# Kernel optimization log

Measured on AMD Instinct MI355X. Metric: run time of the kernel, lower is better.

Reference implementation:

```python
import jax, jax.numpy as jnp
import numpy as np

N_NODES = 100000
N_EDGES = 1600000
C_IN = 128
C_HID = 128
C_OUT = 128


def _gcn_conv(x, row, col, ew, W, b, n_nodes):
    # PyG GCNConv with edge weights and self-loops already included in (row, col, ew).
    # deg[i] = sum of edge weights into node i (flow source->target, aggregate at col)
    xw = x @ W                                                # [N, C_out]
    deg = jax.ops.segment_sum(ew, col, num_segments=n_nodes)  # [N]
    dinv = jnp.where(deg > 0, jax.lax.rsqrt(deg), 0.0)        # deg^{-1/2}, inf -> 0
    norm = dinv[row] * ew * dinv[col]                         # [E]
    msg = xw[row] * norm[:, None]                             # gather + scale
    out = jax.ops.segment_sum(msg, col, num_segments=n_nodes) # scatter-add
    return out + b


def setup_inputs() -> dict:
    key = jax.random.key(0)
    ks = jax.random.split(key, 10)
    x = jax.random.normal(ks[0], (N_NODES, C_IN), dtype=jnp.float32)
    edge_index = jax.random.randint(ks[1], (2, N_EDGES), 0, N_NODES, dtype=jnp.int32)
    edge_weight = jax.random.uniform(ks[2], (N_EDGES,), dtype=jnp.float32)
    s = 1.0 / np.sqrt(C_HID)
    W1 = jax.random.uniform(ks[3], (C_IN, C_HID), minval=-s, maxval=s, dtype=jnp.float32)
    b1 = jnp.zeros((C_HID,), dtype=jnp.float32)
    W2 = jax.random.uniform(ks[4], (C_HID, C_HID), minval=-s, maxval=s, dtype=jnp.float32)
    b2 = jnp.zeros((C_HID,), dtype=jnp.float32)
    W3 = jax.random.uniform(ks[5], (C_HID, C_OUT), minval=-s, maxval=s, dtype=jnp.float32)
    b3 = jnp.zeros((C_OUT,), dtype=jnp.float32)
    return {"x": x, "edge_index": edge_index, "edge_weight": edge_weight,
            "W1": W1, "b1": b1, "W2": W2, "b2": b2, "W3": W3, "b3": b3}


def reference(x, edge_index, edge_weight, W1, b1, W2, b2, W3, b3):
    n = x.shape[0]
    # add self-loops with weight 1 (PyG add_self_loops; identical each layer, built once)
    loop = jnp.arange(n, dtype=edge_index.dtype)
    row = jnp.concatenate([edge_index[0], loop])
    col = jnp.concatenate([edge_index[1], loop])
    ew = jnp.concatenate([edge_weight, jnp.ones((n,), dtype=edge_weight.dtype)])
    h = _gcn_conv(x, row, col, ew, W1, b1, n)
    h = jax.nn.relu(h)
    h = _gcn_conv(h, row, col, ew, W2, b2, n)
    h = jax.nn.relu(h)
    h = _gcn_conv(h, row, col, ew, W3, b3, n)
    return h
```

## Files before the change

### kernel.cpp

```cpp
#include <hip/hip_runtime.h>

#define NN 100000
#define NE 1600000

typedef __attribute__((ext_vector_type(8))) short short8;
typedef __attribute__((ext_vector_type(4))) float f32x4;

static __device__ __forceinline__ unsigned f2bf_rne(float f) {
    unsigned u = __float_as_uint(f);
    return (u + 0x7FFFu + ((u >> 16) & 1u)) >> 16;
}
static __device__ __forceinline__ float bf_lo(unsigned u) { return __uint_as_float(u << 16); }
static __device__ __forceinline__ float bf_hi(unsigned u) { return __uint_as_float(u & 0xFFFF0000u); }

__global__ __launch_bounds__(256) void k_pre(unsigned long long* packed, int n,
                                             const float* __restrict__ W1,
                                             const float* __restrict__ W2,
                                             const float* __restrict__ W3,
                                             ushort* __restrict__ wt) {
    int b = blockIdx.x;
    int t = threadIdx.x;
    if (b < 391) {
        int i = b * 256 + t;
        if (i < n) packed[i] = 0ull;
        return;
    }
    int pb = b - 391;
    int wsel = pb >> 6;
    const float* W = (wsel == 0) ? W1 : (wsel == 1) ? W2 : W3;
    ushort* Wth = wt + wsel * 2 * 16384;
    ushort* Wtl = Wth + 16384;
    int idx = (pb & 63) * 256 + t;
    int k = idx >> 7, nn = idx & 127;
    float w = W[idx];
    unsigned hi = f2bf_rne(w);
    unsigned lo = f2bf_rne(w - bf_lo(hi));
    Wth[nn * 128 + k] = (ushort)hi;
    Wtl[nn * 128 + k] = (ushort)lo;
}

template <bool SPLIT_A>
static __device__ __forceinline__ void mfma_tile(const ushort* sAh, const ushort* sAl,
                                                 const ushort* __restrict__ Wth,
                                                 const ushort* __restrict__ Wtl,
                                                 unsigned* __restrict__ Cb,
                                                 size_t r0, int t) {
    int w  = t >> 6;
    int l  = t & 63;
    int lr = l & 15;
    int lk = (l >> 4) << 3;
    int n0 = w * 32;

    short8 bh[2][4], bl[2][4];
#pragma unroll
    for (int cf = 0; cf < 2; ++cf)
#pragma unroll
        for (int ks = 0; ks < 4; ++ks) {
            int n = n0 + cf * 16 + lr;
            bh[cf][ks] = *(const short8*)&Wth[n * 128 + ks * 32 + lk];
            bl[cf][ks] = *(const short8*)&Wtl[n * 128 + ks * 32 + lk];
        }

    f32x4 zero = {0.f, 0.f, 0.f, 0.f};
    f32x4 acc[2][2] = {{zero, zero}, {zero, zero}};

    __syncthreads();

#pragma unroll
    for (int ks = 0; ks < 4; ++ks) {
        short8 ah[2], al[2];
#pragma unroll
        for (int rf = 0; rf < 2; ++rf) {
            int off = (rf * 16 + lr) * 136 + ks * 32 + lk;
            ah[rf] = *(const short8*)&sAh[off];
            if (SPLIT_A) al[rf] = *(const short8*)&sAl[off];
        }
#pragma unroll
        for (int rf = 0; rf < 2; ++rf)
#pragma unroll
            for (int cf = 0; cf < 2; ++cf) {
                acc[rf][cf] = __builtin_amdgcn_mfma_f32_16x16x32_bf16(ah[rf], bh[cf][ks], acc[rf][cf], 0, 0, 0);
                acc[rf][cf] = __builtin_amdgcn_mfma_f32_16x16x32_bf16(ah[rf], bl[cf][ks], acc[rf][cf], 0, 0, 0);
                if (SPLIT_A)
                    acc[rf][cf] = __builtin_amdgcn_mfma_f32_16x16x32_bf16(al[rf], bh[cf][ks], acc[rf][cf], 0, 0, 0);
            }
    }

#pragma unroll
    for (int rf = 0; rf < 2; ++rf)
#pragma unroll
        for (int cf = 0; cf < 2; ++cf)
#pragma unroll
            for (int r = 0; r < 4; ++r) {
                unsigned b = f2bf_rne(acc[rf][cf][r]);
                unsigned p = (unsigned)__shfl_xor((int)b, 1);
                if (!(l & 1)) {
                    size_t row = r0 + rf * 16 + ((l >> 4) << 2) + r;
                    int c = n0 + cf * 16 + lr;
                    Cb[(row * 128 + c) >> 1] = b | (p << 16);
                }
            }
}

__global__ __launch_bounds__(256) void k_gp(const float* __restrict__ A,
                                            const ushort* __restrict__ Wth,
                                            const ushort* __restrict__ Wtl,
                                            unsigned* __restrict__ Cb,
                                            const int* __restrict__ col,
                                            const float* __restrict__ ew,
                                            unsigned long long* packed,
                                            int* __restrict__ rank, int e) {
    __shared__ alignas(16) ushort sAh[32 * 136];
    __shared__ alignas(16) ushort sAl[32 * 136];
    int b = blockIdx.x;
    int sub = b % 3;
    int q = b / 3;
    int t = threadIdx.x;

    if (sub != 0) {
        int p = q * 2 + sub - 1;
        int i = p * 256 + t;
        if (i < e) {
            int c = col[i];
            unsigned fe = (unsigned)__float2uint_rn(ew[i] * 1048576.0f);
            unsigned long long inc = ((unsigned long long)fe << 24) | 1ull;
            unsigned long long old = atomicAdd(&packed[c], inc);
            rank[i] = (int)(old & 0xFFFFFFull);
        }
        return;
    }

    size_t r0 = (size_t)q * 32;
    const float4* A4 = (const float4*)(A + r0 * 128);
#pragma unroll
    for (int i = 0; i < 4; ++i) {
        int j = t + 256 * i;
        float4 f = A4[j];
        int rr = j >> 5;
        int cc = (j & 31) << 2;
        unsigned h0 = f2bf_rne(f.x), h1 = f2bf_rne(f.y), h2 = f2bf_rne(f.z), h3 = f2bf_rne(f.w);
        unsigned g0 = f2bf_rne(f.x - bf_lo(h0)), g1 = f2bf_rne(f.y - bf_lo(h1));
        unsigned g2 = f2bf_rne(f.z - bf_lo(h2)), g3 = f2bf_rne(f.w - bf_lo(h3));
        *(ushort4*)&sAh[rr * 136 + cc] = make_ushort4((ushort)h0, (ushort)h1, (ushort)h2, (ushort)h3);
        *(ushort4*)&sAl[rr * 136 + cc] = make_ushort4((ushort)g0, (ushort)g1, (ushort)g2, (ushort)g3);
    }
    mfma_tile<true>(sAh, sAl, Wth, Wtl, Cb, r0, t);
}

__global__ __launch_bounds__(256) void k_scan1(const unsigned long long* __restrict__ packed,
                                               int* __restrict__ rowptr,
                                               int* __restrict__ part,
                                               float* __restrict__ dinv, int n) {
    __shared__ int s[256];
    int t = threadIdx.x;
    int i = blockIdx.x * 256 + t;
    unsigned long long pk = (i < n) ? packed[i] : 0ull;
    int v = (int)(pk & 0xFFFFFFull);
    if (i < n) {
        float deg = 1.0f + (float)(pk >> 24) * (1.0f / 1048576.0f);
        dinv[i] = rsqrtf(deg);
    }
    s[t] = v;
    __syncthreads();
    for (int d = 1; d < 256; d <<= 1) {
        int y = (t >= d) ? s[t - d] : 0;
        __syncthreads();
        s[t] += y;
        __syncthreads();
    }
    if (i < n) rowptr[i] = s[t] - v;
    if (t == 255) part[blockIdx.x] = s[255];
}

__global__ __launch_bounds__(512) void k_scan2(int* part, int m) {
    __shared__ int s[512];
    int t = threadIdx.x;
    int v = (t < m) ? part[t] : 0;
    s[t] = v;
    __syncthreads();
    for (int d = 1; d < 512; d <<= 1) {
        int y = (t >= d) ? s[t - d] : 0;
        __syncthreads();
        s[t] += y;
        __syncthreads();
    }
    if (t < m) part[t] = s[t] - v;
}

__global__ __launch_bounds__(256) void k_scan3(int* rowptr, const int* __restrict__ part, int n, int e) {
    int i = blockIdx.x * 256 + threadIdx.x;
    if (i < n) rowptr[i] += part[blockIdx.x];
    if (i == 0) rowptr[n] = e;
}

__global__ __launch_bounds__(256) void k_fill(const int* __restrict__ row,
                                              const int* __restrict__ col,
                                              const float* __restrict__ ew,
                                              const int* __restrict__ rowptr,
                                              const int* __restrict__ rank,
                                              const float* __restrict__ dinv,
                                              uint2* __restrict__ meta, int e) {
    int i = blockIdx.x * 256 + threadIdx.x;
    if (i < e) {
        int c = col[i];
        int r = row[i];
        int p = rowptr[c] + rank[i];
        float w = dinv[r] * ew[i] * dinv[c];
        meta[p] = make_uint2((unsigned)r, __float_as_uint(w));
    }
}

static __device__ __forceinline__ void agg_node(const uint2* __restrict__ X2,
                                                const int* __restrict__ rowptr,
                                                const uint2* __restrict__ meta,
                                                const float* __restrict__ dinv,
                                                const float* __restrict__ bias,
                                                int node, int h, int q,
                                                float& a0, float& a1, float& a2, float& a3) {
    float di = dinv[node];
    float selfw = di * di;
    uint2 us = X2[(size_t)node * 32 + q];
    float4 bv = *(const float4*)(bias + q * 4);
    a0 = fmaf(selfw, bf_lo(us.x), bv.x);
    a1 = fmaf(selfw, bf_hi(us.x), bv.y);
    a2 = fmaf(selfw, bf_lo(us.y), bv.z);
    a3 = fmaf(selfw, bf_hi(us.y), bv.w);

    int p0 = rowptr[node], p1 = rowptr[node + 1];
    int deg = p1 - p0;
    int dmax = max(deg, __shfl_xor(deg, 32));

    for (int base = 0; base < dmax; base += 32) {
        int m = deg - base;
        if (m > 32) m = 32;
        int mm = dmax - base;
        if (mm > 32) mm = 32;
        int idx = p0 + base + (q < m ? q : (m > 0 ? m - 1 : 0));
        if (m <= 0) idx = p0;
        if (idx > NE - 1) idx = NE - 1;
        uint2 mv = meta[idx];
        int sv = (int)mv.x;
        float wv = __uint_as_float(mv.y);

        int j = 0;
        for (; j + 4 <= mm; j += 4) {
#pragma unroll
            for (int u = 0; u < 4; ++u) {
                int jj = j + u;
                int s = __shfl(sv, (h << 5) | jj);
                float w = __shfl(wv, (h << 5) | jj);
                w = (jj < m) ? w : 0.0f;
                uint2 u0 = X2[(size_t)s * 32 + q];
                a0 = fmaf(w, bf_lo(u0.x), a0);  a1 = fmaf(w, bf_hi(u0.x), a1);
                a2 = fmaf(w, bf_lo(u0.y), a2);  a3 = fmaf(w, bf_hi(u0.y), a3);
            }
        }
        for (; j < mm; ++j) {
            int s = __shfl(sv, (h << 5) | j);
            float w = __shfl(wv, (h << 5) | j);
            w = (j < m) ? w : 0.0f;
            uint2 u0 = X2[(size_t)s * 32 + q];
            a0 = fmaf(w, bf_lo(u0.x), a0);  a1 = fmaf(w, bf_hi(u0.x), a1);
            a2 = fmaf(w, bf_lo(u0.y), a2);  a3 = fmaf(w, bf_hi(u0.y), a3);
        }
    }
}

__global__ __launch_bounds__(256) void k_aggemm(const unsigned* __restrict__ Xsrc,
                                                const int* __restrict__ rowptr,
                                                const uint2* __restrict__ meta,
                                                const float* __restrict__ dinv,
                                                const float* __restrict__ bias,
                                                const ushort* __restrict__ Wth,
                                                const ushort* __restrict__ Wtl,
                                                unsigned* __restrict__ Cb) {
    __shared__ alignas(16) ushort sA[32 * 136];
    int t = threadIdx.x;
    int lane = t & 63, wid = t >> 6;
    int h = lane >> 5, q = lane & 31;
    const uint2* X2 = (const uint2*)Xsrc;
    size_t r0 = (size_t)blockIdx.x * 32;

#pragma unroll
    for (int p = 0; p < 4; ++p) {
        int ln = (p << 3) + (wid << 1) + h;
        int node = (int)r0 + ln;
        float a0, a1, a2, a3;
        agg_node(X2, rowptr, meta, dinv, bias, node, h, q, a0, a1, a2, a3);
        a0 = fmaxf(a0, 0.0f);  a1 = fmaxf(a1, 0.0f);
        a2 = fmaxf(a2, 0.0f);  a3 = fmaxf(a3, 0.0f);
        *(ushort4*)&sA[ln * 136 + (q << 2)] =
            make_ushort4((ushort)f2bf_rne(a0), (ushort)f2bf_rne(a1),
                         (ushort)f2bf_rne(a2), (ushort)f2bf_rne(a3));
    }
    mfma_tile<false>(sA, nullptr, Wth, Wtl, Cb, r0, t);
}

__global__ __launch_bounds__(256) void k_agg(const unsigned* __restrict__ XWb,
                                             const int* __restrict__ rowptr,
                                             const uint2* __restrict__ meta,
                                             const float* __restrict__ dinv,
                                             const float* __restrict__ bias,
                                             float* __restrict__ outf, int n) {
    int lane = threadIdx.x & 63;
    int h = lane >> 5;
    int q = lane & 31;
    int node = blockIdx.x * 8 + ((threadIdx.x >> 6) << 1) + h;
    if (node >= n) return;
    float a0, a1, a2, a3;
    agg_node((const uint2*)XWb, rowptr, meta, dinv, bias, node, h, q, a0, a1, a2, a3);
    *(float4*)(outf + (size_t)node * 128 + q * 4) = make_float4(a0, a1, a2, a3);
}

extern "C" void kernel_launch(void* const* d_in, const int* in_sizes, int n_in,
                              void* d_out, int out_size, void* d_ws, size_t ws_size,
                              hipStream_t stream) {
    const float* x  = (const float*)d_in[0];
    const int*   ei = (const int*)d_in[1];
    const float* ew = (const float*)d_in[2];
    const float* W1 = (const float*)d_in[3];
    const float* b1 = (const float*)d_in[4];
    const float* W2 = (const float*)d_in[5];
    const float* b2 = (const float*)d_in[6];
    const float* W3 = (const float*)d_in[7];
    const float* b3 = (const float*)d_in[8];
    float* out = (float*)d_out;

    const int n = NN, e = NE;
    const int* row = ei;
    const int* col = ei + e;

    char* ws = (char*)d_ws;
    size_t off = 0;
    auto alloc = [&](size_t bytes) -> void* {
        void* p = ws + off;
        off = (off + bytes + 255) & ~(size_t)255;
        return p;
    };
    unsigned*           hb     = (unsigned*)alloc((size_t)n * 128 * 2);
    unsigned*           xwb    = (unsigned*)alloc((size_t)n * 128 * 2);
    void*               uni    =            alloc((size_t)e * 8);
    unsigned long long* packed = (unsigned long long*)uni;
    uint2*              meta   = (uint2*)uni;
    float*              dinv   = (float*)   alloc((size_t)n * 4);
    int*                rowptr = (int*)     alloc((size_t)(n + 1) * 4);
    int*                rank   = (int*)     alloc((size_t)e * 4);
    int*                part   = (int*)     alloc(512 * 4);
    ushort*             wt     = (ushort*)  alloc(6 * 16384 * 2);
    (void)ws_size; (void)in_sizes; (void)n_in; (void)out_size;

    int nb = (n + 255) / 256;
    int eb = (e + 255) / 256;
    int gb = n / 32;
    int ab = (n + 7) / 8;

    k_pre<<<nb + 192, 256, 0, stream>>>(packed, n, W1, W2, W3, wt);

    k_gp<<<gb + eb, 256, 0, stream>>>(x, wt + 0 * 16384, wt + 1 * 16384, xwb, col, ew, packed, rank, e);
    k_scan1<<<nb, 256, 0, stream>>>(packed, rowptr, part, dinv, n);
    k_scan2<<<1, 512, 0, stream>>>(part, nb);
    k_scan3<<<nb, 256, 0, stream>>>(rowptr, part, n, e);
    k_fill<<<eb, 256, 0, stream>>>(row, col, ew, rowptr, rank, dinv, meta, e);

    k_aggemm<<<gb, 256, 0, stream>>>(xwb, rowptr, meta, dinv, b1,
                                     wt + 2 * 16384, wt + 3 * 16384, hb);
    k_aggemm<<<gb, 256, 0, stream>>>(hb, rowptr, meta, dinv, b2,
                                     wt + 4 * 16384, wt + 5 * 16384, xwb);
    k_agg<<<ab, 256, 0, stream>>>(xwb, rowptr, meta, dinv, b3, out, n);
}
```

Before: 478.3 us.

## Sort nodes by degree per block and aggregate four nodes per half-wave

Each block of 32 nodes now bitonic-sorts its nodes by in-degree in shared memory. Each half-wave then takes four consecutive sorted nodes and processes them together, interleaving their gathers. This is meant to cut divergence from mismatched degree loops and to keep more independent loads in flight. The separate scan3 kernel is removed: the block offset from part[] is added wherever rowptr is read, at the cost of extra indexed loads, a small sort with several syncs per block, and higher register pressure from 16 accumulators.

```diff
diff --git a/kernel.cpp b/kernel.cpp
--- a/kernel.cpp
+++ b/kernel.cpp
@@ -172,7 +172,7 @@
     if (t == 255) part[blockIdx.x] = s[255];
 }
 
-__global__ __launch_bounds__(512) void k_scan2(int* part, int m) {
+__global__ __launch_bounds__(512) void k_scan2(int* part, int m, int* rowptr, int e) {
     __shared__ int s[512];
     int t = threadIdx.x;
     int v = (t < m) ? part[t] : 0;
@@ -185,18 +185,14 @@
         __syncthreads();
     }
     if (t < m) part[t] = s[t] - v;
-}
-
-__global__ __launch_bounds__(256) void k_scan3(int* rowptr, const int* __restrict__ part, int n, int e) {
-    int i = blockIdx.x * 256 + threadIdx.x;
-    if (i < n) rowptr[i] += part[blockIdx.x];
-    if (i == 0) rowptr[n] = e;
+    if (t == m - 1) rowptr[NN] = e - (s[t] - v);
 }
 
 __global__ __launch_bounds__(256) void k_fill(const int* __restrict__ row,
                                               const int* __restrict__ col,
                                               const float* __restrict__ ew,
                                               const int* __restrict__ rowptr,
+                                              const int* __restrict__ part,
                                               const int* __restrict__ rank,
                                               const float* __restrict__ dinv,
                                               uint2* __restrict__ meta, int e) {
@@ -204,70 +200,123 @@
     if (i < e) {
         int c = col[i];
         int r = row[i];
-        int p = rowptr[c] + rank[i];
+        int p = rowptr[c] + part[c >> 8] + rank[i];
         float w = dinv[r] * ew[i] * dinv[c];
         meta[p] = make_uint2((unsigned)r, __float_as_uint(w));
     }
 }
 
-static __device__ __forceinline__ void agg_node(const uint2* __restrict__ X2,
-                                                const int* __restrict__ rowptr,
+static __device__ __forceinline__ void agg_quad(const uint2* __restrict__ X2,
                                                 const uint2* __restrict__ meta,
                                                 const float* __restrict__ dinv,
-                                                const float* __restrict__ bias,
-                                                int node, int h, int q,
-                                                float& a0, float& a1, float& a2, float& a3) {
-    float di = dinv[node];
-    float selfw = di * di;
-    uint2 us = X2[(size_t)node * 32 + q];
-    float4 bv = *(const float4*)(bias + q * 4);
-    a0 = fmaf(selfw, bf_lo(us.x), bv.x);
-    a1 = fmaf(selfw, bf_hi(us.x), bv.y);
-    a2 = fmaf(selfw, bf_lo(us.y), bv.z);
-    a3 = fmaf(selfw, bf_hi(us.y), bv.w);
-
-    int p0 = rowptr[node], p1 = rowptr[node + 1];
-    int deg = p1 - p0;
-    int dmax = max(deg, __shfl_xor(deg, 32));
-
-    for (int base = 0; base < dmax; base += 32) {
-        int m = deg - base;
-        if (m > 32) m = 32;
-        int mm = dmax - base;
-        if (mm > 32) mm = 32;
-        int idx = p0 + base + (q < m ? q : (m > 0 ? m - 1 : 0));
-        if (m <= 0) idx = p0;
-        if (idx > NE - 1) idx = NE - 1;
-        uint2 mv = meta[idx];
-        int sv = (int)mv.x;
-        float wv = __uint_as_float(mv.y);
+                                                float4 bv, int h, int q,
+                                                const int* node, const int* p0,
+                                                const int* deg, float acc[4][4]) {
+#pragma unroll
+    for (int X = 0; X < 4; ++X) {
+        float di = dinv[node[X]];
+        float sw = di * di;
+        uint2 us = X2[(size_t)node[X] * 32 + q];
+        acc[X][0] = fmaf(sw, bf_lo(us.x), bv.x);
+        acc[X][1] = fmaf(sw, bf_hi(us.x), bv.y);
+        acc[X][2] = fmaf(sw, bf_lo(us.y), bv.z);
+        acc[X][3] = fmaf(sw, bf_hi(us.y), bv.w);
+    }
+    int dloc = max(max(deg[0], deg[1]), max(deg[2], deg[3]));
+
+    for (int base = 0; base < dloc; base += 32) {
+        int m[4], idx[4];
+#pragma unroll
+        for (int X = 0; X < 4; ++X) {
+            int mx = deg[X] - base;
+            m[X] = mx > 32 ? 32 : mx;
+            int ix = p0[X] + base + (q < m[X] ? q : (m[X] > 0 ? m[X] - 1 : 0));
+            if (m[X] <= 0) ix = p0[X];
+            if (ix > NE - 1) ix = NE - 1;
+            idx[X] = ix;
+        }
+        int sv[4]; float wv[4];
+#pragma unroll
+        for (int X = 0; X < 4; ++X) {
+            uint2 mv = meta[idx[X]];
+            sv[X] = (int)mv.x;
+            wv[X] = __uint_as_float(mv.y);
+        }
+        int mmax = dloc - base;  mmax = mmax > 32 ? 32 : mmax;
 
         int j = 0;
-        for (; j + 4 <= mm; j += 4) {
+        for (; j + 4 <= mmax; j += 4) {
 #pragma unroll
             for (int u = 0; u < 4; ++u) {
                 int jj = j + u;
-                int s = __shfl(sv, (h << 5) | jj);
-                float w = __shfl(wv, (h << 5) | jj);
-                w = (jj < m) ? w : 0.0f;
-                uint2 u0 = X2[(size_t)s * 32 + q];
-                a0 = fmaf(w, bf_lo(u0.x), a0);  a1 = fmaf(w, bf_hi(u0.x), a1);
-                a2 = fmaf(w, bf_lo(u0.y), a2);  a3 = fmaf(w, bf_hi(u0.y), a3);
+#pragma unroll
+                for (int X = 0; X < 4; ++X) {
+                    int s = __shfl(sv[X], (h << 5) | jj);
+                    float w = __shfl(wv[X], (h << 5) | jj);
+                    w = (jj < m[X]) ? w : 0.0f;
+                    uint2 ux = X2[(size_t)s * 32 + q];
+                    acc[X][0] = fmaf(w, bf_lo(ux.x), acc[X][0]);
+                    acc[X][1] = fmaf(w, bf_hi(ux.x), acc[X][1]);
+                    acc[X][2] = fmaf(w, bf_lo(ux.y), acc[X][2]);
+                    acc[X][3] = fmaf(w, bf_hi(ux.y), acc[X][3]);
+                }
             }
         }
-        for (; j < mm; ++j) {
-            int s = __shfl(sv, (h << 5) | j);
-            float w = __shfl(wv, (h << 5) | j);
-            w = (j < m) ? w : 0.0f;
-            uint2 u0 = X2[(size_t)s * 32 + q];
-            a0 = fmaf(w, bf_lo(u0.x), a0);  a1 = fmaf(w, bf_hi(u0.x), a1);
-            a2 = fmaf(w, bf_lo(u0.y), a2);  a3 = fmaf(w, bf_hi(u0.y), a3);
-        }
+        for (; j < mmax; ++j) {
+#pragma unroll
+            for (int X = 0; X < 4; ++X) {
+                int s = __shfl(sv[X], (h << 5) | j);
+                float w = __shfl(wv[X], (h << 5) | j);
+                w = (j < m[X]) ? w : 0.0f;
+                uint2 ux = X2[(size_t)s * 32 + q];
+                acc[X][0] = fmaf(w, bf_lo(ux.x), acc[X][0]);
+                acc[X][1] = fmaf(w, bf_hi(ux.x), acc[X][1]);
+                acc[X][2] = fmaf(w, bf_lo(ux.y), acc[X][2]);
+                acc[X][3] = fmaf(w, bf_hi(ux.y), acc[X][3]);
+            }
+        }
+    }
+}
+
+static __device__ __forceinline__ void sort_and_assign(const int* __restrict__ rowptr,
+                                                       const int* __restrict__ part,
+                                                       size_t r0, int t, int g,
+                                                       int* skey,
+                                                       int* node, int* p0, int* deg, int* ln) {
+    if (t < 32) {
+        int i = (int)r0 + t;
+        int pa = rowptr[i] + part[i >> 8];
+        int pb = rowptr[i + 1] + part[(i + 1) >> 8];
+        skey[t] = ((pb - pa) << 5) | t;
+    }
+    __syncthreads();
+    for (int k = 2; k <= 32; k <<= 1) {
+        for (int s = k >> 1; s > 0; s >>= 1) {
+            if (t < 32) {
+                int ixj = t ^ s;
+                if (ixj > t) {
+                    int a = skey[t], b = skey[ixj];
+                    bool asc = ((t & k) == 0);
+                    if (asc ? (a > b) : (a < b)) { skey[t] = b; skey[ixj] = a; }
+                }
+            }
+            __syncthreads();
+        }
+    }
+#pragma unroll
+    for (int s = 0; s < 4; ++s) {
+        int key = skey[g * 4 + s];
+        ln[s] = key & 31;
+        deg[s] = key >> 5;
+        int i = (int)r0 + ln[s];
+        node[s] = i;
+        p0[s] = rowptr[i] + part[i >> 8];
     }
 }
 
 __global__ __launch_bounds__(256) void k_aggemm(const unsigned* __restrict__ Xsrc,
                                                 const int* __restrict__ rowptr,
+                                                const int* __restrict__ part,
                                                 const uint2* __restrict__ meta,
                                                 const float* __restrict__ dinv,
                                                 const float* __restrict__ bias,
@@ -275,21 +324,26 @@
                                                 const ushort* __restrict__ Wtl,
                                                 unsigned* __restrict__ Cb) {
     __shared__ alignas(16) ushort sA[32 * 136];
+    __shared__ int skey[32];
     int t = threadIdx.x;
     int lane = t & 63, wid = t >> 6;
     int h = lane >> 5, q = lane & 31;
+    int g = (wid << 1) | h;
     const uint2* X2 = (const uint2*)Xsrc;
     size_t r0 = (size_t)blockIdx.x * 32;
 
-#pragma unroll
-    for (int p = 0; p < 4; ++p) {
-        int ln = (p << 3) + (wid << 1) + h;
-        int node = (int)r0 + ln;
-        float a0, a1, a2, a3;
-        agg_node(X2, rowptr, meta, dinv, bias, node, h, q, a0, a1, a2, a3);
-        a0 = fmaxf(a0, 0.0f);  a1 = fmaxf(a1, 0.0f);
-        a2 = fmaxf(a2, 0.0f);  a3 = fmaxf(a3, 0.0f);
-        *(ushort4*)&sA[ln * 136 + (q << 2)] =
+    int node[4], p0[4], deg[4], ln[4];
+    sort_and_assign(rowptr, part, r0, t, g, skey, node, p0, deg, ln);
+
+    float4 bv = *(const float4*)(bias + q * 4);
+    float acc[4][4];
+    agg_quad(X2, meta, dinv, bv, h, q, node, p0, deg, acc);
+
+#pragma unroll
+    for (int X = 0; X < 4; ++X) {
+        float a0 = fmaxf(acc[X][0], 0.0f), a1 = fmaxf(acc[X][1], 0.0f);
+        float a2 = fmaxf(acc[X][2], 0.0f), a3 = fmaxf(acc[X][3], 0.0f);
+        *(ushort4*)&sA[ln[X] * 136 + (q << 2)] =
             make_ushort4((ushort)f2bf_rne(a0), (ushort)f2bf_rne(a1),
                          (ushort)f2bf_rne(a2), (ushort)f2bf_rne(a3));
     }
@@ -298,18 +352,29 @@
 
 __global__ __launch_bounds__(256) void k_agg(const unsigned* __restrict__ XWb,
                                              const int* __restrict__ rowptr,
+                                             const int* __restrict__ part,
                                              const uint2* __restrict__ meta,
                                              const float* __restrict__ dinv,
                                              const float* __restrict__ bias,
-                                             float* __restrict__ outf, int n) {
-    int lane = threadIdx.x & 63;
-    int h = lane >> 5;
-    int q = lane & 31;
-    int node = blockIdx.x * 8 + ((threadIdx.x >> 6) << 1) + h;
-    if (node >= n) return;
-    float a0, a1, a2, a3;
-    agg_node((const uint2*)XWb, rowptr, meta, dinv, bias, node, h, q, a0, a1, a2, a3);
-    *(float4*)(outf + (size_t)node * 128 + q * 4) = make_float4(a0, a1, a2, a3);
+                                             float* __restrict__ outf) {
+    __shared__ int skey[32];
+    int t = threadIdx.x;
+    int lane = t & 63, wid = t >> 6;
+    int h = lane >> 5, q = lane & 31;
+    int g = (wid << 1) | h;
+    size_t r0 = (size_t)blockIdx.x * 32;
+
+    int node[4], p0[4], deg[4], ln[4];
+    sort_and_assign(rowptr, part, r0, t, g, skey, node, p0, deg, ln);
+
+    float4 bv = *(const float4*)(bias + q * 4);
+    float acc[4][4];
+    agg_quad((const uint2*)XWb, meta, dinv, bv, h, q, node, p0, deg, acc);
+
+#pragma unroll
+    for (int X = 0; X < 4; ++X)
+        *(float4*)(outf + (size_t)node[X] * 128 + q * 4) =
+            make_float4(acc[X][0], acc[X][1], acc[X][2], acc[X][3]);
 }
 
 extern "C" void kernel_launch(void* const* d_in, const int* in_sizes, int n_in,
@@ -352,19 +417,17 @@
     int nb = (n + 255) / 256;
     int eb = (e + 255) / 256;
     int gb = n / 32;
-    int ab = (n + 7) / 8;
 
     k_pre<<<nb + 192, 256, 0, stream>>>(packed, n, W1, W2, W3, wt);
 
     k_gp<<<gb + eb, 256, 0, stream>>>(x, wt + 0 * 16384, wt + 1 * 16384, xwb, col, ew, packed, rank, e);
     k_scan1<<<nb, 256, 0, stream>>>(packed, rowptr, part, dinv, n);
-    k_scan2<<<1, 512, 0, stream>>>(part, nb);
-    k_scan3<<<nb, 256, 0, stream>>>(rowptr, part, n, e);
-    k_fill<<<eb, 256, 0, stream>>>(row, col, ew, rowptr, rank, dinv, meta, e);
-
-    k_aggemm<<<gb, 256, 0, stream>>>(xwb, rowptr, meta, dinv, b1,
+    k_scan2<<<1, 512, 0, stream>>>(part, nb, rowptr, e);
+    k_fill<<<eb, 256, 0, stream>>>(row, col, ew, rowptr, part, rank, dinv, meta, e);
+
+    k_aggemm<<<gb, 256, 0, stream>>>(xwb, rowptr, part, meta, dinv, b1,
                                      wt + 2 * 16384, wt + 3 * 16384, hb);
-    k_aggemm<<<gb, 256, 0, stream>>>(hb, rowptr, meta, dinv, b2,
+    k_aggemm<<<gb, 256, 0, stream>>>(hb, rowptr, part, meta, dinv, b2,
                                      wt + 4 * 16384, wt + 5 * 16384, xwb);
-    k_agg<<<ab, 256, 0, stream>>>(xwb, rowptr, meta, dinv, b3, out, n);
-}
+    k_agg<<<gb, 256, 0, stream>>>(xwb, rowptr, part, meta, dinv, b3, out);
+}
```

Measured after the change: 522.9 us. +9.3%, slower.
